# Kernel optimization log

Hardware: AMD Instinct MI355X
Metric: run time of the kernel (lower is better)

The kernel has to match this reference:

```python
import jax, jax.numpy as jnp
import numpy as np

N_NODES = 100000
N_EDGES = 1600000
NUM_GRAPHS = 1024
D_IN = 128
D_HID = 128
D_OUT = 2
LN_EPS = 1e-5


def setup_inputs() -> dict:
    key = jax.random.key(0)
    ks = jax.random.split(key, 10)
    x = jax.random.normal(ks[0], (N_NODES, D_IN), dtype=jnp.float32)
    edge_index = jax.random.randint(ks[1], (2, N_EDGES), 0, N_NODES, dtype=jnp.int64)
    batch = jnp.sort(jax.random.randint(ks[2], (N_NODES,), 0, NUM_GRAPHS, dtype=jnp.int64))
    s = 0.05  # weight scale to keep activations sane
    return {
        "x": x,
        "edge_index": edge_index,
        "batch": batch,
        "W1l": jax.random.normal(ks[3], (D_HID, D_IN), dtype=jnp.float32) * s,
        "b1l": jnp.zeros((D_HID,), dtype=jnp.float32),
        "W1r": jax.random.normal(ks[4], (D_HID, D_IN), dtype=jnp.float32) * s,
        "W2l": jax.random.normal(ks[5], (D_HID, D_HID), dtype=jnp.float32) * s,
        "b2l": jnp.zeros((D_HID,), dtype=jnp.float32),
        "W2r": jax.random.normal(ks[6], (D_HID, D_HID), dtype=jnp.float32) * s,
        "ln_g": jnp.ones((D_HID,), dtype=jnp.float32),
        "ln_b": jnp.zeros((D_HID,), dtype=jnp.float32),
        "Wlin": jax.random.normal(ks[7], (D_OUT, D_HID), dtype=jnp.float32) * s,
        "blin": jnp.zeros((D_OUT,), dtype=jnp.float32),
    }


def _sage_conv(x, src, dst, Wl, bl, Wr):
    # PyG SAGEConv with mean aggregation: lin_l(mean_{j in N(i)} x_j) + lin_r(x_i)
    msg_sum = jax.ops.segment_sum(x[src], dst, num_segments=N_NODES)
    deg = jax.ops.segment_sum(jnp.ones((src.shape[0], 1), x.dtype), dst, num_segments=N_NODES)
    agg = msg_sum / jnp.maximum(deg, 1.0)  # isolated nodes -> 0
    return agg @ Wl.T + bl + x @ Wr.T  # lin_r has no bias (PyG default)


def reference(x, edge_index, batch, W1l, b1l, W1r, W2l, b2l, W2r, ln_g, ln_b, Wlin, blin):
    src, dst = edge_index[0], edge_index[1]
    h = jax.nn.relu(_sage_conv(x, src, dst, W1l, b1l, W1r))
    h = jax.nn.relu(_sage_conv(h, src, dst, W2l, b2l, W2r))
    # global_add_pool over graphs
    g = jax.ops.segment_sum(h, batch, num_segments=NUM_GRAPHS)  # [G, D_HID]
    # LayerNorm over last dim
    mu = jnp.mean(g, axis=-1, keepdims=True)
    var = jnp.var(g, axis=-1, keepdims=True)
    gn = (g - mu) * jax.lax.rsqrt(var + LN_EPS) * ln_g + ln_b
    return gn @ Wlin.T + blin  # [G, D_OUT]
```

## Files before the change

### kernel.cpp

```cpp
#include <hip/hip_runtime.h>
#include <hip/hip_bf16.h>

#define N_NODES   100000
#define N_EDGES   1600000
#define NUM_GRAPHS 1024
#define D         128
#define LN_EPS    1e-5f
#define NBUCKETS  391
#define CAP       4864
#define CHUNK     4096

typedef __attribute__((ext_vector_type(8))) short short8;
typedef __attribute__((ext_vector_type(4))) float floatx4;
typedef __attribute__((ext_vector_type(2))) float f32x2;

static __device__ __forceinline__ float bf2f(unsigned int u) {
    return __uint_as_float(u << 16);
}
static __device__ __forceinline__ unsigned short f2bf(float f) {
    __hip_bfloat16 h = __float2bfloat16(f);
    return *reinterpret_cast<unsigned short*>(&h);
}
static __device__ __forceinline__ void acc4(f32x2* acc, uint4 v) {
    acc[0] += (f32x2){__uint_as_float(v.x << 16), __uint_as_float(v.x & 0xffff0000u)};
    acc[1] += (f32x2){__uint_as_float(v.y << 16), __uint_as_float(v.y & 0xffff0000u)};
    acc[2] += (f32x2){__uint_as_float(v.z << 16), __uint_as_float(v.z & 0xffff0000u)};
    acc[3] += (f32x2){__uint_as_float(v.w << 16), __uint_as_float(v.w & 0xffff0000u)};
}

__global__ __launch_bounds__(256)
void prep_kernel(const float* __restrict__ x, unsigned short* __restrict__ xbf,
                 const float* __restrict__ W1l, const float* __restrict__ W1r,
                 const float* __restrict__ W2l, const float* __restrict__ W2r,
                 unsigned short* __restrict__ Wc1, unsigned short* __restrict__ Wc2,
                 int* __restrict__ cursor) {
    int i = blockIdx.x * 256 + threadIdx.x;
    float4 v = reinterpret_cast<const float4*>(x)[i];
    ushort4 o;
    o.x = f2bf(v.x); o.y = f2bf(v.y); o.z = f2bf(v.z); o.w = f2bf(v.w);
    reinterpret_cast<ushort4*>(xbf)[i] = o;
    if (blockIdx.x < 256) {
        int layer = i >> 15;
        int rem = i & 32767;
        int c = rem >> 8;
        int k = rem & 255;
        const float* Wl = layer ? W2l : W1l;
        const float* Wr = layer ? W2r : W1r;
        unsigned short* dst = layer ? Wc2 : Wc1;
        float wv = (k < 128) ? Wl[c * 128 + k] : Wr[c * 128 + (k - 128)];
        dst[c * 256 + k] = f2bf(wv);
    }
    if (blockIdx.x == 256) {
        for (int b = threadIdx.x; b < NBUCKETS; b += 256)
            cursor[b] = b * CAP;
    }
}

__global__ __launch_bounds__(256)
void bin_scatter_kernel(const int* __restrict__ src, const int* __restrict__ dst,
                        int* __restrict__ cursor, unsigned* __restrict__ binned) {
    __shared__ int cnt[NBUCKETS];
    __shared__ int base[NBUCKETS];
    int chunkBase = blockIdx.x * CHUNK;
    for (int i = threadIdx.x; i < NBUCKETS; i += 256) cnt[i] = 0;
    __syncthreads();
    int es[16], ed[16], lofs[16];
    #pragma unroll
    for (int j = 0; j < 16; ++j) {
        int e = chunkBase + j * 256 + threadIdx.x;
        if (e < N_EDGES) {
            es[j] = src[e];
            ed[j] = dst[e];
            lofs[j] = atomicAdd(&cnt[ed[j] >> 8], 1);
        }
    }
    __syncthreads();
    for (int i = threadIdx.x; i < NBUCKETS; i += 256) {
        int c = cnt[i];
        base[i] = c ? atomicAdd(&cursor[i], c) : 0;
    }
    __syncthreads();
    #pragma unroll
    for (int j = 0; j < 16; ++j) {
        int e = chunkBase + j * 256 + threadIdx.x;
        if (e < N_EDGES) {
            int b = ed[j] >> 8;
            int pos = base[b] + lofs[j];
            if (pos < (b + 1) * CAP)
                binned[pos] = ((unsigned)(ed[j] & 255) << 17) | (unsigned)es[j];
        }
    }
}

__global__ __launch_bounds__(256)
void bucket_build_kernel(const unsigned* __restrict__ binned, const int* __restrict__ cursor,
                         int2* __restrict__ row_info, int* __restrict__ src_sorted) {
    __shared__ int scnt[256];
    __shared__ int sscan[256];
    int b = blockIdx.x;
    int t = threadIdx.x;
    int lo = b * CAP;
    int hi = cursor[b];
    int cap_end = lo + CAP;
    if (hi > cap_end) hi = cap_end;
    scnt[t] = 0;
    __syncthreads();
    unsigned rec[19];
    short rnk[19];
    #pragma unroll
    for (int i = 0; i < 19; ++i) {
        int e = lo + t + i * 256;
        if (e < hi) {
            unsigned r = binned[e];
            rec[i] = r;
            rnk[i] = (short)atomicAdd(&scnt[r >> 17], 1);
        }
    }
    __syncthreads();
    int v = scnt[t];
    sscan[t] = v;
    __syncthreads();
    for (int off = 1; off < 256; off <<= 1) {
        int a = (t >= off) ? sscan[t - off] : 0;
        __syncthreads();
        sscan[t] += a;
        __syncthreads();
    }
    int ex = sscan[t] - v;
    int node = b * 256 + t;
    if (node < N_NODES) row_info[node] = make_int2(lo + ex, v);
    scnt[t] = ex;
    __syncthreads();
    #pragma unroll
    for (int i = 0; i < 19; ++i) {
        int e = lo + t + i * 256;
        if (e < hi) {
            unsigned r = rec[i];
            src_sorted[lo + scnt[r >> 17] + rnk[i]] = (int)(r & 0x1FFFFu);
        }
    }
}

__global__ __launch_bounds__(256)
void aggregate_kernel(const unsigned short* __restrict__ feat,
                      const int* __restrict__ src_sorted,
                      const int2* __restrict__ row_info,
                      unsigned short* __restrict__ aggout) {
    int wave = threadIdx.x >> 6;
    int lane = threadIdx.x & 63;
    int node = blockIdx.x * 4 + wave;
    int sub = lane >> 4;
    int ch = (lane & 15) * 8;
    int2 ri = row_info[node];
    int s = ri.x, deg = ri.y;
    const unsigned short* fb = feat + ch;
    f32x2 acc[4];
    acc[0] = acc[1] = acc[2] = acc[3] = (f32x2){0.f, 0.f};

    if (deg <= 64) {
        int si = 0;
        if (lane < deg) si = src_sorted[s + lane];
        int rounds = (deg + 3) >> 2;
        for (int r = 0; r < rounds; ++r) {
            int eidx = r * 4 + sub;
            int u = __shfl(si, eidx, 64);
            if (eidx < deg) {
                uint4 v = *(const uint4*)(fb + (size_t)u * 128);
                acc4(acc, v);
            }
        }
    } else {
        for (int j = s + sub; j < s + deg; j += 4) {
            int u = src_sorted[j];
            uint4 v = *(const uint4*)(fb + (size_t)u * 128);
            acc4(acc, v);
        }
    }
    #pragma unroll
    for (int i = 0; i < 4; ++i) {
        acc[i].x += __shfl_xor(acc[i].x, 16, 64);
        acc[i].y += __shfl_xor(acc[i].y, 16, 64);
        acc[i].x += __shfl_xor(acc[i].x, 32, 64);
        acc[i].y += __shfl_xor(acc[i].y, 32, 64);
    }
    float inv = 1.f / (float)(deg > 1 ? deg : 1);
    if (sub == 0) {
        uint4 ov;
        ov.x = (unsigned)f2bf(acc[0].x * inv) | ((unsigned)f2bf(acc[0].y * inv) << 16);
        ov.y = (unsigned)f2bf(acc[1].x * inv) | ((unsigned)f2bf(acc[1].y * inv) << 16);
        ov.z = (unsigned)f2bf(acc[2].x * inv) | ((unsigned)f2bf(acc[2].y * inv) << 16);
        ov.w = (unsigned)f2bf(acc[3].x * inv) | ((unsigned)f2bf(acc[3].y * inv) << 16);
        *(uint4*)(aggout + (size_t)node * 128 + ch) = ov;
    }
}

__global__ __launch_bounds__(256)
void gemm_kernel(const unsigned short* __restrict__ A1,
                 const unsigned short* __restrict__ A2,
                 const unsigned short* __restrict__ Wcat,
                 const float* __restrict__ bias,
                 unsigned short* __restrict__ out) {
    __shared__ unsigned short Asm[64][32];
    __shared__ unsigned short Wsm[128][32];
    int tid = threadIdx.x;
    int wave = tid >> 6;
    int lane = tid & 63;
    int nodeBase = blockIdx.x * 64;
    floatx4 acc[4][2];
    #pragma unroll
    for (int a = 0; a < 4; ++a)
        #pragma unroll
        for (int b = 0; b < 2; ++b) acc[a][b] = (floatx4){0.f, 0.f, 0.f, 0.f};

    int r = tid >> 2, sg = tid & 3;
    int quad = lane >> 4, m = lane & 15;

    for (int kc = 0; kc < 8; ++kc) {
        const unsigned short* Asrc = (kc < 4) ? A1 : A2;
        int kOff = (kc & 3) * 32;
        int node = nodeBase + r;
        float4 av = make_float4(0.f, 0.f, 0.f, 0.f);
        if (node < N_NODES) av = *(const float4*)(Asrc + (size_t)node * 128 + kOff + sg * 8);
        *(float4*)(&Asm[r][sg * 8]) = av;
        #pragma unroll
        for (int it = 0; it < 2; ++it) {
            int idx = tid + it * 256;
            int wr = idx >> 2, wsg = idx & 3;
            *(float4*)(&Wsm[wr][wsg * 8]) = *(const float4*)(Wcat + wr * 256 + kc * 32 + wsg * 8);
        }
        __syncthreads();
        short8 afr[4], bfr[2];
        #pragma unroll
        for (int nb = 0; nb < 4; ++nb)
            afr[nb] = *(const short8*)(&Asm[nb * 16 + m][quad * 8]);
        #pragma unroll
        for (int cb = 0; cb < 2; ++cb)
            bfr[cb] = *(const short8*)(&Wsm[wave * 32 + cb * 16 + m][quad * 8]);
        #pragma unroll
        for (int nb = 0; nb < 4; ++nb)
            #pragma unroll
            for (int cb = 0; cb < 2; ++cb)
                acc[nb][cb] = __builtin_amdgcn_mfma_f32_16x16x32_bf16(afr[nb], bfr[cb], acc[nb][cb], 0, 0, 0);
        __syncthreads();
    }
    #pragma unroll
    for (int cb = 0; cb < 2; ++cb) {
        int col = wave * 32 + cb * 16 + m;
        float bv = bias[col];
        #pragma unroll
        for (int nb = 0; nb < 4; ++nb) {
            #pragma unroll
            for (int rr = 0; rr < 4; ++rr) {
                int row = nodeBase + nb * 16 + quad * 4 + rr;
                if (row < N_NODES) {
                    float v = acc[nb][cb][rr] + bv;
                    v = v > 0.f ? v : 0.f;
                    out[(size_t)row * 128 + col] = f2bf(v);
                }
            }
        }
    }
}

__global__ __launch_bounds__(256)
void pool_ln_out_kernel(const unsigned short* __restrict__ h2,
                        const int* __restrict__ batch,
                        const float* __restrict__ ln_g, const float* __restrict__ ln_b,
                        const float* __restrict__ Wlin, const float* __restrict__ blin,
                        float* __restrict__ out) {
    int g = blockIdx.x;
    int t = threadIdx.x;
    int lane = t & 63, w = t >> 6;
    __shared__ int se[2];
    if (t < 2) {
        int target = g + t;
        int lo = 0, hi = N_NODES;
        while (lo < hi) {
            int mid = (lo + hi) >> 1;
            if (batch[mid] < target) lo = mid + 1; else hi = mid;
        }
        se[t] = lo;
    }
    __syncthreads();
    int s = se[0], e = se[1];
    int ns = t >> 4;
    int chg = t & 15;
    f32x2 a[4];
    a[0] = a[1] = a[2] = a[3] = (f32x2){0.f, 0.f};
    for (int n = s + ns; n < e; n += 16) {
        uint4 v = *(const uint4*)(h2 + (size_t)n * 128 + chg * 8);
        acc4(a, v);
    }
    #pragma unroll
    for (int i = 0; i < 4; ++i) {
        a[i].x += __shfl_xor(a[i].x, 16, 64);
        a[i].y += __shfl_xor(a[i].y, 16, 64);
        a[i].x += __shfl_xor(a[i].x, 32, 64);
        a[i].y += __shfl_xor(a[i].y, 32, 64);
    }
    __shared__ float sw[4][128];
    if (lane < 16) {
        #pragma unroll
        for (int k = 0; k < 4; ++k) {
            sw[w][chg * 8 + 2 * k]     = a[k].x;
            sw[w][chg * 8 + 2 * k + 1] = a[k].y;
        }
    }
    __syncthreads();
    __shared__ float red[128];
    float sum = 0.f;
    if (t < 128) {
        sum = sw[0][t] + sw[1][t] + sw[2][t] + sw[3][t];
        red[t] = sum;
    }
    __syncthreads();
    for (int off = 64; off > 0; off >>= 1) {
        if (t < off) red[t] += red[t + off];
        __syncthreads();
    }
    float mu = red[0] * (1.f / 128.f);
    __syncthreads();
    float dv = sum - mu;
    if (t < 128) red[t] = dv * dv;
    __syncthreads();
    for (int off = 64; off > 0; off >>= 1) {
        if (t < off) red[t] += red[t + off];
        __syncthreads();
    }
    float var = red[0] * (1.f / 128.f);
    __syncthreads();
    __shared__ float r0[128], r1[128];
    if (t < 128) {
        float gn = dv * rsqrtf(var + LN_EPS) * ln_g[t] + ln_b[t];
        r0[t] = gn * Wlin[t];
        r1[t] = gn * Wlin[128 + t];
    }
    __syncthreads();
    for (int off = 64; off > 0; off >>= 1) {
        if (t < off) { r0[t] += r0[t + off]; r1[t] += r1[t + off]; }
        __syncthreads();
    }
    if (t == 0) {
        out[g * 2 + 0] = r0[0] + blin[0];
        out[g * 2 + 1] = r1[0] + blin[1];
    }
}

extern "C" void kernel_launch(void* const* d_in, const int* in_sizes, int n_in,
                              void* d_out, int out_size, void* d_ws, size_t ws_size,
                              hipStream_t stream) {
    const float* x    = (const float*)d_in[0];
    const int*   ei   = (const int*)d_in[1];
    const int*   batch= (const int*)d_in[2];
    const float* W1l  = (const float*)d_in[3];
    const float* b1l  = (const float*)d_in[4];
    const float* W1r  = (const float*)d_in[5];
    const float* W2l  = (const float*)d_in[6];
    const float* b2l  = (const float*)d_in[7];
    const float* W2r  = (const float*)d_in[8];
    const float* ln_g = (const float*)d_in[9];
    const float* ln_b = (const float*)d_in[10];
    const float* Wlin = (const float*)d_in[11];
    const float* blin = (const float*)d_in[12];
    float* out = (float*)d_out;

    char* ws = (char*)d_ws;
    size_t off = 0;
    auto alloc = [&](size_t bytes) {
        char* p = ws + off;
        off = (off + bytes + 255) & ~(size_t)255;
        return p;
    };
    unsigned short* xbf  = (unsigned short*)alloc((size_t)N_NODES * D * 2);
    unsigned short* aggb = (unsigned short*)alloc((size_t)N_NODES * D * 2);
    unsigned short* h1   = (unsigned short*)alloc((size_t)N_NODES * D * 2);
    unsigned short* Wc1  = (unsigned short*)alloc(128 * 256 * 2);
    unsigned short* Wc2  = (unsigned short*)alloc(128 * 256 * 2);
    int2* row_info   = (int2*)alloc((size_t)N_NODES * 8);
    int* src_sorted  = (int*)alloc((size_t)NBUCKETS * CAP * 4);
    int* cursor      = (int*)alloc(NBUCKETS * 4);
    unsigned* binned = (unsigned*)aggb;

    const int* srcI = ei;
    const int* dstI = ei + N_EDGES;

    prep_kernel<<<12500, 256, 0, stream>>>(x, xbf, W1l, W1r, W2l, W2r, Wc1, Wc2, cursor);
    bin_scatter_kernel<<<(N_EDGES + CHUNK - 1) / CHUNK, 256, 0, stream>>>(srcI, dstI, cursor, binned);
    bucket_build_kernel<<<NBUCKETS, 256, 0, stream>>>(binned, cursor, row_info, src_sorted);

    aggregate_kernel<<<25000, 256, 0, stream>>>(xbf, src_sorted, row_info, aggb);
    gemm_kernel<<<1563, 256, 0, stream>>>(aggb, xbf, Wc1, b1l, h1);
    aggregate_kernel<<<25000, 256, 0, stream>>>(h1, src_sorted, row_info, aggb);
    gemm_kernel<<<1563, 256, 0, stream>>>(aggb, h1, Wc2, b2l, xbf);
    pool_ln_out_kernel<<<NUM_GRAPHS, 256, 0, stream>>>(xbf, batch, ln_g, ln_b, Wlin, blin, out);
}
```

Before: 329.5 us.

## Preload full A tile and weights in registers, drop per-k-chunk syncs

The GEMM kernel now loads the whole 64x256 A tile (both aggregated and self features) into padded shared memory in one pass and keeps each wave's weight fragments in registers, read straight from global memory. This removes the eight-step loop that restaged A and W through LDS with two barriers per step, leaving a single barrier. The padded row stride is meant to avoid LDS bank conflicts. In exchange it uses more LDS (about 36KB per block) and more registers per thread for the weight fragments, which may lower occupancy.

```diff
diff --git a/kernel.cpp b/kernel.cpp
--- a/kernel.cpp
+++ b/kernel.cpp
@@ -9,6 +9,7 @@
 #define NBUCKETS  391
 #define CAP       4864
 #define CHUNK     4096
+#define ASTRIDE   288
 
 typedef __attribute__((ext_vector_type(8))) short short8;
 typedef __attribute__((ext_vector_type(4))) float floatx4;
@@ -200,48 +201,54 @@
                  const unsigned short* __restrict__ Wcat,
                  const float* __restrict__ bias,
                  unsigned short* __restrict__ out) {
-    __shared__ unsigned short Asm[64][32];
-    __shared__ unsigned short Wsm[128][32];
+    __shared__ unsigned short Asm[64][ASTRIDE];
     int tid = threadIdx.x;
     int wave = tid >> 6;
     int lane = tid & 63;
+    int quad = lane >> 4, m = lane & 15;
     int nodeBase = blockIdx.x * 64;
-    floatx4 acc[4][2];
-    #pragma unroll
-    for (int a = 0; a < 4; ++a)
-        #pragma unroll
-        for (int b = 0; b < 2; ++b) acc[a][b] = (floatx4){0.f, 0.f, 0.f, 0.f};
-
-    int r = tid >> 2, sg = tid & 3;
-    int quad = lane >> 4, m = lane & 15;
-
-    for (int kc = 0; kc < 8; ++kc) {
-        const unsigned short* Asrc = (kc < 4) ? A1 : A2;
-        int kOff = (kc & 3) * 32;
+
+    short8 bfr[8][2];
+    #pragma unroll
+    for (int kc = 0; kc < 8; ++kc)
+        #pragma unroll
+        for (int cb = 0; cb < 2; ++cb)
+            bfr[kc][cb] = *(const short8*)(Wcat + (size_t)(wave * 32 + cb * 16 + m) * 256 + kc * 32 + quad * 8);
+
+    #pragma unroll
+    for (int it = 0; it < 8; ++it) {
+        int i = it * 256 + tid;
+        int r = i >> 5;
+        int c8 = i & 31;
         int node = nodeBase + r;
         float4 av = make_float4(0.f, 0.f, 0.f, 0.f);
-        if (node < N_NODES) av = *(const float4*)(Asrc + (size_t)node * 128 + kOff + sg * 8);
-        *(float4*)(&Asm[r][sg * 8]) = av;
-        #pragma unroll
-        for (int it = 0; it < 2; ++it) {
-            int idx = tid + it * 256;
-            int wr = idx >> 2, wsg = idx & 3;
-            *(float4*)(&Wsm[wr][wsg * 8]) = *(const float4*)(Wcat + wr * 256 + kc * 32 + wsg * 8);
-        }
-        __syncthreads();
-        short8 afr[4], bfr[2];
+        if (node < N_NODES) {
+            const unsigned short* srcp = (c8 < 16)
+                ? (A1 + (size_t)node * 128 + c8 * 8)
+                : (A2 + (size_t)node * 128 + (c8 - 16) * 8);
+            av = *(const float4*)srcp;
+        }
+        *(float4*)(&Asm[r][c8 * 8]) = av;
+    }
+    __syncthreads();
+
+    floatx4 acc[4][2];
+    #pragma unroll
+    for (int a = 0; a < 4; ++a)
+        #pragma unroll
+        for (int b = 0; b < 2; ++b) acc[a][b] = (floatx4){0.f, 0.f, 0.f, 0.f};
+
+    #pragma unroll
+    for (int kc = 0; kc < 8; ++kc) {
+        short8 afr[4];
         #pragma unroll
         for (int nb = 0; nb < 4; ++nb)
-            afr[nb] = *(const short8*)(&Asm[nb * 16 + m][quad * 8]);
-        #pragma unroll
-        for (int cb = 0; cb < 2; ++cb)
-            bfr[cb] = *(const short8*)(&Wsm[wave * 32 + cb * 16 + m][quad * 8]);
+            afr[nb] = *(const short8*)(&Asm[nb * 16 + m][kc * 32 + quad * 8]);
         #pragma unroll
         for (int nb = 0; nb < 4; ++nb)
             #pragma unroll
             for (int cb = 0; cb < 2; ++cb)
-                acc[nb][cb] = __builtin_amdgcn_mfma_f32_16x16x32_bf16(afr[nb], bfr[cb], acc[nb][cb], 0, 0, 0);
-        __syncthreads();
+                acc[nb][cb] = __builtin_amdgcn_mfma_f32_16x16x32_bf16(afr[nb], bfr[kc][cb], acc[nb][cb], 0, 0, 0);
     }
     #pragma unroll
     for (int cb = 0; cb < 2; ++cb) {
```

Result: slower. 350.2 us (+6.3%).
